# Kernel tuning notes

Measured on AMD Instinct MI355X. Metric: run time of the kernel, lower is better.

The kernel has to match this reference:

```python
import jax, jax.numpy as jnp
import numpy as np

B, T, H, S, K, V = 64, 2048, 512, 512, 128, 128
EPS = 1e-12  # F.normalize default eps


def setup_inputs() -> dict:
    key = jax.random.key(0)
    ks = jax.random.split(key, 9)
    scale_s = 1.0 / np.sqrt(S)
    scale_h = 1.0 / np.sqrt(H)
    return {
        "decoder_state": jax.random.normal(ks[0], (B, S), jnp.float32),
        "listener_output": jax.random.normal(ks[1], (B, T, H), jnp.float32),
        "outputs_length": jax.random.randint(ks[2], (B,), 1, T + 1, jnp.int32),
        "Ws": jax.random.uniform(ks[3], (K, S), jnp.float32, -scale_s, scale_s),
        "bs": jax.random.uniform(ks[4], (K,), jnp.float32, -scale_s, scale_s),
        "Wh": jax.random.uniform(ks[5], (K, H), jnp.float32, -scale_h, scale_h),
        "bh": jax.random.uniform(ks[6], (K,), jnp.float32, -scale_h, scale_h),
        "Wv": jax.random.uniform(ks[7], (V, H), jnp.float32, -scale_h, scale_h),
        "bv": jax.random.uniform(ks[8], (V,), jnp.float32, -scale_h, scale_h),
    }


def reference(decoder_state, listener_output, outputs_length, Ws, bs, Wh, bh, Wv, bv):
    # query: (B, K); key: (B, T, K)
    query = decoder_state @ Ws.T + bs
    keys = jnp.einsum('bth,kh->btk', listener_output, Wh) + bh
    energy = jnp.einsum('bk,btk->bt', query, keys)          # (B, T)
    attention = jax.nn.softmax(energy, axis=-1)
    # mask: positions >= outputs_length[i] zeroed, EXCEPT sample i == 0 (original loop skips i==0)
    t_idx = jnp.arange(T)
    valid = t_idx[None, :] < outputs_length[:, None]        # (B, T)
    valid = valid.at[0].set(True)
    mask = valid.astype(attention.dtype)
    attention = attention * mask
    # L1 normalize over time (F.normalize p=1, dim=2)
    denom = jnp.maximum(jnp.sum(jnp.abs(attention), axis=-1, keepdims=True), EPS)
    attention = attention / denom
    value = jnp.einsum('bth,vh->btv', listener_output, Wv) + bv  # (B, T, V)
    value = value * mask[:, :, None]
    context = jnp.einsum('bt,btv->bv', attention, value)     # (B, V)
    return context, attention[:, None, :]
```

## Files before the change

### kernel.cpp

```cpp
#include <hip/hip_runtime.h>
#include <hip/hip_bf16.h>

#define B 64
#define T 2048
#define H 512
#define S 512
#define K 128
#define V 128
#define SPL 16
#define RPB (T / SPL)
#define RPW (RPB / 4)
#define PSTRIDE 516

__global__ __launch_bounds__(256) void prep_kernel(
    const float* __restrict__ dec, const float* __restrict__ Ws,
    const float* __restrict__ bs, const float* __restrict__ Wh,
    const float* __restrict__ bh, float* __restrict__ wq,
    float* __restrict__ cb) {
  const int b = blockIdx.x;
  const int tid = threadIdx.x;
  __shared__ float s_dec[S];
  __shared__ float s_q[K];

  for (int i = tid; i < S; i += 256) s_dec[i] = dec[b * S + i];
  __syncthreads();

  if (tid < K) {
    const float* w = Ws + (size_t)tid * S;
    float acc = bs[tid];
    #pragma unroll 4
    for (int s = 0; s < S; s++) acc += w[s] * s_dec[s];
    s_q[tid] = acc;
  }
  __syncthreads();

  if (tid == 0) {
    float c = 0.f;
    for (int k = 0; k < K; k++) c += s_q[k] * bh[k];
    cb[b] = c;
  }
  for (int h = tid; h < H; h += 256) {
    float acc = 0.f;
    #pragma unroll 4
    for (int k = 0; k < K; k++) acc += s_q[k] * Wh[(size_t)k * H + h];
    wq[b * H + h] = acc;
  }
}

__global__ __launch_bounds__(256) void fused_kernel(
    const float* __restrict__ L, const float* __restrict__ wq,
    const float* __restrict__ cb, const int* __restrict__ len,
    float* __restrict__ energy, float* __restrict__ partials) {
  const int b = blockIdx.x >> 4;
  const int sp = blockIdx.x & (SPL - 1);
  const int lane = threadIdx.x & 63;
  const int wave = threadIdx.x >> 6;
  const int tid = threadIdx.x;
  const int lb = (b == 0) ? T : len[b];

  __shared__ float s_ctx[4][H];
  __shared__ float s_ml[4][2];

  const int h0 = lane * 4;
  float m = -__builtin_huge_valf();
  float lsum = 0.f;
  float4 acc0 = {0.f, 0.f, 0.f, 0.f};
  float4 acc1 = {0.f, 0.f, 0.f, 0.f};

  const int start = sp * RPB + wave * RPW;
  const int end = min(start + RPW, lb);

  if (start < end) {
    const float4 q0 = *(const float4*)(wq + b * H + h0);
    const float4 q1 = *(const float4*)(wq + b * H + 256 + h0);
    const float c = cb[b];
    const float* Lr = L + ((size_t)b * T + start) * H;
    for (int r = start; r < end; r++, Lr += H) {
      const float4 a0 = *(const float4*)(Lr + h0);
      const float4 a1 = *(const float4*)(Lr + 256 + h0);
      float d = a0.x * q0.x + a0.y * q0.y + a0.z * q0.z + a0.w * q0.w +
                a1.x * q1.x + a1.y * q1.y + a1.z * q1.z + a1.w * q1.w;
      #pragma unroll
      for (int off = 32; off > 0; off >>= 1) d += __shfl_xor(d, off);
      const float e = d + c;
      if (lane == 0) energy[b * T + r] = e;
      if (e > m) {
        const float s = __expf(m - e);
        lsum *= s;
        acc0.x *= s; acc0.y *= s; acc0.z *= s; acc0.w *= s;
        acc1.x *= s; acc1.y *= s; acc1.z *= s; acc1.w *= s;
        m = e;
      }
      const float w = __expf(e - m);
      lsum += w;
      acc0.x += w * a0.x; acc0.y += w * a0.y;
      acc0.z += w * a0.z; acc0.w += w * a0.w;
      acc1.x += w * a1.x; acc1.y += w * a1.y;
      acc1.z += w * a1.z; acc1.w += w * a1.w;
    }
  }

  if (lane == 0) { s_ml[wave][0] = m; s_ml[wave][1] = lsum; }
  *(float4*)&s_ctx[wave][h0] = acc0;
  *(float4*)&s_ctx[wave][256 + h0] = acc1;
  __syncthreads();

  const float M = fmaxf(fmaxf(s_ml[0][0], s_ml[1][0]),
                        fmaxf(s_ml[2][0], s_ml[3][0]));
  float sc[4], ltot = 0.f;
  #pragma unroll
  for (int w = 0; w < 4; w++) {
    sc[w] = (s_ml[w][0] > -1e38f) ? __expf(s_ml[w][0] - M) : 0.f;
    ltot += s_ml[w][1] * sc[w];
  }
  float v0 = 0.f, v1 = 0.f;
  #pragma unroll
  for (int w = 0; w < 4; w++) {
    v0 += s_ctx[w][tid * 2] * sc[w];
    v1 += s_ctx[w][tid * 2 + 1] * sc[w];
  }
  float* part = partials + (size_t)blockIdx.x * PSTRIDE;
  *(float2*)(part + tid * 2) = make_float2(v0, v1);
  if (tid == 0) { part[512] = M; part[513] = ltot; }
}

__global__ __launch_bounds__(256) void combine_kernel(
    const float* __restrict__ partials, const float* __restrict__ Wv,
    const float* __restrict__ bv, float* __restrict__ ctx_out,
    float* __restrict__ Mv, float* __restrict__ Iv) {
  const int b = blockIdx.x;
  const int tid = threadIdx.x;
  __shared__ float s_ml[SPL][2];
  __shared__ float s_ctx[H];

  if (tid < SPL) {
    const float* p = partials + (size_t)(b * SPL + tid) * PSTRIDE;
    s_ml[tid][0] = p[512];
    s_ml[tid][1] = p[513];
  }
  __syncthreads();

  float M = -__builtin_huge_valf();
  #pragma unroll
  for (int sp = 0; sp < SPL; sp++) M = fmaxf(M, s_ml[sp][0]);
  float sc[SPL], ltot = 0.f;
  #pragma unroll
  for (int sp = 0; sp < SPL; sp++) {
    sc[sp] = (s_ml[sp][0] > -1e38f) ? __expf(s_ml[sp][0] - M) : 0.f;
    ltot += s_ml[sp][1] * sc[sp];
  }
  const float inv = 1.0f / fmaxf(ltot, 1e-12f);

  float v0 = 0.f, v1 = 0.f;
  #pragma unroll 4
  for (int sp = 0; sp < SPL; sp++) {
    const float* p = partials + (size_t)(b * SPL + sp) * PSTRIDE;
    v0 += p[tid * 2] * sc[sp];
    v1 += p[tid * 2 + 1] * sc[sp];
  }
  s_ctx[tid * 2] = v0 * inv;
  s_ctx[tid * 2 + 1] = v1 * inv;
  if (tid == 0) { Mv[b] = M; Iv[b] = inv; }
  __syncthreads();

  if (tid < V) {
    const float* w = Wv + (size_t)tid * H;
    float a = bv[tid];
    #pragma unroll 4
    for (int h = 0; h < H; h += 4) {
      a += w[h] * s_ctx[h] + w[h + 1] * s_ctx[h + 1] +
           w[h + 2] * s_ctx[h + 2] + w[h + 3] * s_ctx[h + 3];
    }
    ctx_out[b * V + tid] = a;
  }
}

__global__ __launch_bounds__(256) void attwrite_kernel(
    const float* __restrict__ energy, const int* __restrict__ len,
    const float* __restrict__ Mv, const float* __restrict__ Iv,
    float* __restrict__ att) {
  const int b = blockIdx.x;
  const int tid = threadIdx.x;
  const int lb = (b == 0) ? T : len[b];
  const float M = Mv[b];
  const float inv = Iv[b];
  #pragma unroll
  for (int i = 0; i < 8; i++) {
    const int t = tid + 256 * i;
    const float e = (t < lb) ? energy[b * T + t] : M;
    att[b * T + t] = (t < lb) ? __expf(e - M) * inv : 0.f;
  }
}

extern "C" void kernel_launch(void* const* d_in, const int* in_sizes, int n_in,
                              void* d_out, int out_size, void* d_ws,
                              size_t ws_size, hipStream_t stream) {
  const float* dec = (const float*)d_in[0];
  const float* L   = (const float*)d_in[1];
  const int*   len = (const int*)d_in[2];
  const float* Ws  = (const float*)d_in[3];
  const float* bs  = (const float*)d_in[4];
  const float* Wh  = (const float*)d_in[5];
  const float* bh  = (const float*)d_in[6];
  const float* Wv  = (const float*)d_in[7];
  const float* bv  = (const float*)d_in[8];

  float* ctx_out = (float*)d_out;
  float* att_out = (float*)d_out + B * V;

  float* ws = (float*)d_ws;
  float* wq = ws;
  float* cb = wq + B * H;
  float* energy = cb + B;
  float* partials = energy + B * T;
  float* Mv = partials + B * SPL * PSTRIDE;
  float* Iv = Mv + B;

  prep_kernel<<<B, 256, 0, stream>>>(dec, Ws, bs, Wh, bh, wq, cb);
  fused_kernel<<<B * SPL, 256, 0, stream>>>(L, wq, cb, len, energy, partials);
  combine_kernel<<<B, 256, 0, stream>>>(partials, Wv, bv, ctx_out, Mv, Iv);
  attwrite_kernel<<<B, 256, 0, stream>>>(energy, len, Mv, Iv, att_out);
}
```

Before: 421.7 us.

## Double split count, unroll online softmax by two, fuse attention write into combine

```diff
diff --git a/kernel.cpp b/kernel.cpp
--- a/kernel.cpp
+++ b/kernel.cpp
@@ -7,7 +7,7 @@
 #define S 512
 #define K 128
 #define V 128
-#define SPL 16
+#define SPL 32
 #define RPB (T / SPL)
 #define RPW (RPB / 4)
 #define PSTRIDE 516
@@ -29,7 +29,11 @@
     const float* w = Ws + (size_t)tid * S;
     float acc = bs[tid];
     #pragma unroll 4
-    for (int s = 0; s < S; s++) acc += w[s] * s_dec[s];
+    for (int s = 0; s < S; s += 4) {
+      const float4 wv = *(const float4*)(w + s);
+      const float4 dv = *(const float4*)(s_dec + s);
+      acc += wv.x * dv.x + wv.y * dv.y + wv.z * dv.z + wv.w * dv.w;
+    }
     s_q[tid] = acc;
   }
   __syncthreads();
@@ -51,7 +55,7 @@
     const float* __restrict__ L, const float* __restrict__ wq,
     const float* __restrict__ cb, const int* __restrict__ len,
     float* __restrict__ energy, float* __restrict__ partials) {
-  const int b = blockIdx.x >> 4;
+  const int b = blockIdx.x >> 5;
   const int sp = blockIdx.x & (SPL - 1);
   const int lane = threadIdx.x & 63;
   const int wave = threadIdx.x >> 6;
@@ -75,7 +79,43 @@
     const float4 q1 = *(const float4*)(wq + b * H + 256 + h0);
     const float c = cb[b];
     const float* Lr = L + ((size_t)b * T + start) * H;
-    for (int r = start; r < end; r++, Lr += H) {
+    int r = start;
+    for (; r + 1 < end; r += 2, Lr += 2 * H) {
+      const float4 a0 = *(const float4*)(Lr + h0);
+      const float4 a1 = *(const float4*)(Lr + 256 + h0);
+      const float4 b0 = *(const float4*)(Lr + H + h0);
+      const float4 b1 = *(const float4*)(Lr + H + 256 + h0);
+      float d0 = a0.x * q0.x + a0.y * q0.y + a0.z * q0.z + a0.w * q0.w +
+                 a1.x * q1.x + a1.y * q1.y + a1.z * q1.z + a1.w * q1.w;
+      float d1 = b0.x * q0.x + b0.y * q0.y + b0.z * q0.z + b0.w * q0.w +
+                 b1.x * q1.x + b1.y * q1.y + b1.z * q1.z + b1.w * q1.w;
+      #pragma unroll
+      for (int off = 32; off > 0; off >>= 1) {
+        d0 += __shfl_xor(d0, off);
+        d1 += __shfl_xor(d1, off);
+      }
+      const float e0 = d0 + c;
+      const float e1 = d1 + c;
+      if (lane == 0) {
+        energy[b * T + r] = e0;
+        energy[b * T + r + 1] = e1;
+      }
+      const float mn = fmaxf(m, fmaxf(e0, e1));
+      const float s = __expf(m - mn);
+      const float w0 = __expf(e0 - mn);
+      const float w1 = __expf(e1 - mn);
+      m = mn;
+      lsum = lsum * s + w0 + w1;
+      acc0.x = acc0.x * s + w0 * a0.x + w1 * b0.x;
+      acc0.y = acc0.y * s + w0 * a0.y + w1 * b0.y;
+      acc0.z = acc0.z * s + w0 * a0.z + w1 * b0.z;
+      acc0.w = acc0.w * s + w0 * a0.w + w1 * b0.w;
+      acc1.x = acc1.x * s + w0 * a1.x + w1 * b1.x;
+      acc1.y = acc1.y * s + w0 * a1.y + w1 * b1.y;
+      acc1.z = acc1.z * s + w0 * a1.z + w1 * b1.z;
+      acc1.w = acc1.w * s + w0 * a1.w + w1 * b1.w;
+    }
+    if (r < end) {
       const float4 a0 = *(const float4*)(Lr + h0);
       const float4 a1 = *(const float4*)(Lr + 256 + h0);
       float d = a0.x * q0.x + a0.y * q0.y + a0.z * q0.z + a0.w * q0.w +
@@ -84,19 +124,19 @@
       for (int off = 32; off > 0; off >>= 1) d += __shfl_xor(d, off);
       const float e = d + c;
       if (lane == 0) energy[b * T + r] = e;
-      if (e > m) {
-        const float s = __expf(m - e);
-        lsum *= s;
-        acc0.x *= s; acc0.y *= s; acc0.z *= s; acc0.w *= s;
-        acc1.x *= s; acc1.y *= s; acc1.z *= s; acc1.w *= s;
-        m = e;
-      }
-      const float w = __expf(e - m);
-      lsum += w;
-      acc0.x += w * a0.x; acc0.y += w * a0.y;
-      acc0.z += w * a0.z; acc0.w += w * a0.w;
-      acc1.x += w * a1.x; acc1.y += w * a1.y;
-      acc1.z += w * a1.z; acc1.w += w * a1.w;
+      const float mn = fmaxf(m, e);
+      const float s = __expf(m - mn);
+      const float w = __expf(e - mn);
+      m = mn;
+      lsum = lsum * s + w;
+      acc0.x = acc0.x * s + w * a0.x;
+      acc0.y = acc0.y * s + w * a0.y;
+      acc0.z = acc0.z * s + w * a0.z;
+      acc0.w = acc0.w * s + w * a0.w;
+      acc1.x = acc1.x * s + w * a1.x;
+      acc1.y = acc1.y * s + w * a1.y;
+      acc1.z = acc1.z * s + w * a1.z;
+      acc1.w = acc1.w * s + w * a1.w;
     }
   }
 
@@ -126,8 +166,9 @@
 
 __global__ __launch_bounds__(256) void combine_kernel(
     const float* __restrict__ partials, const float* __restrict__ Wv,
-    const float* __restrict__ bv, float* __restrict__ ctx_out,
-    float* __restrict__ Mv, float* __restrict__ Iv) {
+    const float* __restrict__ bv, const float* __restrict__ energy,
+    const int* __restrict__ len, float* __restrict__ ctx_out,
+    float* __restrict__ att) {
   const int b = blockIdx.x;
   const int tid = threadIdx.x;
   __shared__ float s_ml[SPL][2];
@@ -143,25 +184,33 @@
   float M = -__builtin_huge_valf();
   #pragma unroll
   for (int sp = 0; sp < SPL; sp++) M = fmaxf(M, s_ml[sp][0]);
-  float sc[SPL], ltot = 0.f;
+  float ltot = 0.f;
   #pragma unroll
   for (int sp = 0; sp < SPL; sp++) {
-    sc[sp] = (s_ml[sp][0] > -1e38f) ? __expf(s_ml[sp][0] - M) : 0.f;
-    ltot += s_ml[sp][1] * sc[sp];
+    const float s = (s_ml[sp][0] > -1e38f) ? __expf(s_ml[sp][0] - M) : 0.f;
+    ltot += s_ml[sp][1] * s;
   }
   const float inv = 1.0f / fmaxf(ltot, 1e-12f);
 
   float v0 = 0.f, v1 = 0.f;
   #pragma unroll 4
   for (int sp = 0; sp < SPL; sp++) {
+    const float s = (s_ml[sp][0] > -1e38f) ? __expf(s_ml[sp][0] - M) : 0.f;
     const float* p = partials + (size_t)(b * SPL + sp) * PSTRIDE;
-    v0 += p[tid * 2] * sc[sp];
-    v1 += p[tid * 2 + 1] * sc[sp];
+    v0 += p[tid * 2] * s;
+    v1 += p[tid * 2 + 1] * s;
   }
   s_ctx[tid * 2] = v0 * inv;
   s_ctx[tid * 2 + 1] = v1 * inv;
-  if (tid == 0) { Mv[b] = M; Iv[b] = inv; }
-  __syncthreads();
+  __syncthreads();
+
+  const int lb = (b == 0) ? T : len[b];
+  #pragma unroll
+  for (int i = 0; i < 8; i++) {
+    const int t = tid + 256 * i;
+    const float e = (t < lb) ? energy[b * T + t] : M;
+    att[b * T + t] = (t < lb) ? __expf(e - M) * inv : 0.f;
+  }
 
   if (tid < V) {
     const float* w = Wv + (size_t)tid * H;
@@ -172,23 +221,6 @@
            w[h + 2] * s_ctx[h + 2] + w[h + 3] * s_ctx[h + 3];
     }
     ctx_out[b * V + tid] = a;
-  }
-}
-
-__global__ __launch_bounds__(256) void attwrite_kernel(
-    const float* __restrict__ energy, const int* __restrict__ len,
-    const float* __restrict__ Mv, const float* __restrict__ Iv,
-    float* __restrict__ att) {
-  const int b = blockIdx.x;
-  const int tid = threadIdx.x;
-  const int lb = (b == 0) ? T : len[b];
-  const float M = Mv[b];
-  const float inv = Iv[b];
-  #pragma unroll
-  for (int i = 0; i < 8; i++) {
-    const int t = tid + 256 * i;
-    const float e = (t < lb) ? energy[b * T + t] : M;
-    att[b * T + t] = (t < lb) ? __expf(e - M) * inv : 0.f;
   }
 }
 
@@ -213,11 +245,9 @@
   float* cb = wq + B * H;
   float* energy = cb + B;
   float* partials = energy + B * T;
-  float* Mv = partials + B * SPL * PSTRIDE;
-  float* Iv = Mv + B;
 
   prep_kernel<<<B, 256, 0, stream>>>(dec, Ws, bs, Wh, bh, wq, cb);
   fused_kernel<<<B * SPL, 256, 0, stream>>>(L, wq, cb, len, energy, partials);
-  combine_kernel<<<B, 256, 0, stream>>>(partials, Wv, bv, ctx_out, Mv, Iv);
-  attwrite_kernel<<<B, 256, 0, stream>>>(energy, len, Mv, Iv, att_out);
-}
+  combine_kernel<<<B, 256, 0, stream>>>(partials, Wv, bv, energy, len,
+                                        ctx_out, att_out);
+}
```

Measured after the change: 416.0 us. No clear change (-1.3%).
